# Kernel optimization log

Measured on AMD Instinct MI355X. Metric: run time of the kernel, lower is better.

## Reference

```python
import jax, jax.numpy as jnp
import numpy as np

N, F, H, CLS = 50000, 64, 128, 64   # nodes, node_features, second_features, num_classes
E, EL = 800000, 200000              # graph edges, decode (label) edges


def setup_inputs() -> dict:
    key = jax.random.key(0)
    ks = jax.random.split(key, 12)
    sc = lambda k, sh, fan: (jax.random.normal(k, sh, jnp.float32) / np.sqrt(fan)).astype(jnp.float32)
    return dict(
        x=jax.random.normal(ks[0], (N, F), jnp.float32),
        edge_index=jax.random.randint(ks[1], (2, E), 0, N),
        edge_label_index=jax.random.randint(ks[2], (2, EL), 0, N),
        hidden1=jnp.zeros((N, H), jnp.float32),   # H state of GCLSTM
        hidden2=jnp.zeros((N, H), jnp.float32),   # C state of GCLSTM
        # GCNConv params
        W_gcn=sc(ks[3], (F, F), F),
        b_gcn=jnp.zeros((F,), jnp.float32),
        # GCLSTM params, gates stacked along last axis in order (i, f, c, o)
        Wx=sc(ks[4], (F, 4 * H), F),      # input->gate weights W_i..W_o
        Th=sc(ks[5], (H, 4 * H), H),      # ChebConv(K=1) thetas on H (pure linear)
        b_gate=jnp.zeros((4 * H,), jnp.float32),  # b_i, b_f, b_c, b_o
        b_conv=jnp.zeros((4 * H,), jnp.float32),  # ChebConv biases
        w_c=sc(ks[6], (3, H), H),         # peephole w_c_i, w_c_f, w_c_o
        # output Linear
        W_lin=sc(ks[7], (H, CLS), H),
        b_lin=jnp.zeros((CLS,), jnp.float32),
    )


def _gcn(x, src, dst, W, b, n):
    """PyG GCNConv: add self-loops, symmetric D^-1/2 (A+I) D^-1/2 normalization."""
    xw = x @ W                                   # [N,F]
    loop = jnp.arange(n)
    src = jnp.concatenate([src, loop])
    dst = jnp.concatenate([dst, loop])
    deg = jax.ops.segment_sum(jnp.ones(src.shape, jnp.float32), dst, num_segments=n)
    dinv = jnp.where(deg > 0, jax.lax.rsqrt(deg), 0.0)
    norm = dinv[src] * dinv[dst]                 # [E+N]
    agg = jax.ops.segment_sum(norm[:, None] * xw[src], dst, num_segments=n)
    return agg + b


def reference(x, edge_index, edge_label_index, hidden1, hidden2,
              W_gcn, b_gcn, Wx, Th, b_gate, b_conv, w_c, W_lin, b_lin):
    n = x.shape[0]
    h = _gcn(x, edge_index[0], edge_index[1], W_gcn, b_gcn, n)   # GCNConv  [N,F]
    # GCLSTM, K=1: ChebConv on H degenerates to H @ Theta + b_conv
    g = (h @ Wx + b_gate) + (hidden1 @ Th + b_conv)              # [N,4H]
    gi, gf, gc, go = jnp.split(g, 4, axis=1)
    I = jax.nn.sigmoid(gi + w_c[0] * hidden2)
    Fg = jax.nn.sigmoid(gf + w_c[1] * hidden2)
    C = Fg * hidden2 + I * jnp.tanh(gc)
    O = jax.nn.sigmoid(go + w_c[2] * C)          # peephole on NEW cell state
    Hn = O * jnp.tanh(C)                         # [N,H]
    z = jax.nn.softmax(jax.nn.relu(Hn) @ W_lin + b_lin, axis=1)  # [N,CLS]
    # decode: dot product of endpoint embeddings
    r = jnp.sum(z[edge_label_index[0]] * z[edge_label_index[1]], axis=-1)  # [EL]
    # faithful to the original forward: returns input hidden1 and the NEW cell state
    return (r, hidden1, C)
```

## Files before the change

kernel.cpp:

```cpp
#include <hip/hip_runtime.h>
#include <math.h>

#define FDIM 64
#define HDIM 128
#define CLSD 64

#define NPART 8
#define MAXDEG 64

typedef unsigned short ushort_t;
typedef _Float16 hfrag __attribute__((ext_vector_type(8)));
typedef float f32x4 __attribute__((ext_vector_type(4)));

#define LOG2E 1.4426950408889634f

__device__ __forceinline__ float ex2(float x){ float r; asm("v_exp_f32 %0, %1" : "=v"(r) : "v"(x)); return r; }
__device__ __forceinline__ float rcp_(float x){ float r; asm("v_rcp_f32 %0, %1" : "=v"(r) : "v"(x)); return r; }
__device__ __forceinline__ float fsigmoid(float x){ return rcp_(1.0f + ex2(-LOG2E*x)); }
__device__ __forceinline__ float ftanh(float x){ return 1.0f - 2.0f*rcp_(1.0f + ex2(2.0f*LOG2E*x)); }

__device__ __forceinline__ ushort_t f2h(float f){
    _Float16 h = (_Float16)f;
    ushort_t u; __builtin_memcpy(&u, &h, 2); return u;
}
__device__ __forceinline__ float hflo(unsigned int u){
    ushort_t v = (ushort_t)u; _Float16 h; __builtin_memcpy(&h, &v, 2); return (float)h;
}
__device__ __forceinline__ float hfhi(unsigned int u){
    ushort_t v = (ushort_t)(u >> 16); _Float16 h; __builtin_memcpy(&h, &v, 2); return (float)h;
}
__device__ __forceinline__ unsigned int pk2h(float a, float b){
    return (unsigned int)f2h(a) | ((unsigned int)f2h(b) << 16);
}


__launch_bounds__(256)
__global__ void k_pre(const float* __restrict__ x,  const float* __restrict__ Wg,
                      const float* __restrict__ bg,
                      const float* __restrict__ Wx, const float* __restrict__ Th,
                      const float* __restrict__ Wl,
                      const float* __restrict__ bga, const float* __restrict__ bco,
                      const float* __restrict__ h1, const int* __restrict__ ei,
                      ushort_t* __restrict__ Bh, ushort_t* __restrict__ Lh,
                      float* __restrict__ bsum, int* __restrict__ cnt,
                      int* __restrict__ ell,
                      ushort_t* __restrict__ xh, ushort_t* __restrict__ Ab,
                      float* __restrict__ oh1, int N, int N2, int E, int psz,
                      int epBlocks){
    int t = threadIdx.x;
    if ((int)blockIdx.x < epBlocks){
        int p   = blockIdx.x % NPART;
        int bi  = blockIdx.x / NPART;
        int bpp = epBlocks / NPART;
        int chunk = (E + bpp - 1) / bpp;
        int beg = bi*chunk;
        int end = beg + chunk; if (end > E) end = E;
        int lo = p*psz, hi = lo + psz;
        for (int i = beg + t; i < end; i += 256){
            int d = ei[E + i];
            if (d >= lo && d < hi){
                int s = ei[i];
                int slot = atomicAdd(&cnt[d], 1);
                if (slot < MAXDEG) ell[(size_t)d*MAXDEG + slot] = s;
            }
        }
        return;
    }
    int tid = ((int)blockIdx.x - epBlocks)*256 + t;
    const int secX = 107008 + N*8;
    if (tid < 98304){
        int k = tid >> 9, col = tid & 511;
        float v;
        if (k < 64){
            float acc = 0.f;
            #pragma unroll 8
            for (int f = 0; f < 64; ++f) acc += Wg[k*64 + f]*Wx[f*512 + col];
            v = acc;
        } else {
            v = Th[(k-64)*512 + col];
        }
        int g = col >> 7, hc = col & 127;
        int w = hc >> 5, within = hc & 31;
        int c8 = g*2 + (within >> 4);
        int T = w*8 + c8;
        int s = k >> 5;
        int lane = ((k >> 3) & 3)*16 + (within & 15);
        int pos = ((T*6 + s)*64 + lane)*8 + (k & 7);
        Bh[pos] = f2h(v);
    } else if (tid < 106496){
        int i = tid - 98304;
        int k = i >> 6, col = i & 63;
        float v = Wl[k*64 + col];
        int ct = col >> 4;
        int s = k >> 5;
        int lane = ((k >> 3) & 3)*16 + (col & 15);
        int pos = ((ct*4 + s)*64 + lane)*8 + (k & 7);
        Lh[pos] = f2h(v);
    } else if (tid < 107008){
        int c = tid - 106496;
        float acc = bga[c] + bco[c];
        #pragma unroll 8
        for (int f = 0; f < 64; ++f) acc += bg[f]*Wx[f*512 + c];
        bsum[c] = acc;
    } else if (tid < secX){
        int i = tid - 107008;
        const float4* xp = (const float4*)(x + (size_t)i*8);
        float4 p0 = xp[0], p1 = xp[1];
        ((int4*)xh)[i] = make_int4((int)pk2h(p0.x,p0.y), (int)pk2h(p0.z,p0.w),
                                   (int)pk2h(p1.x,p1.y), (int)pk2h(p1.z,p1.w));
    } else {
        int i = tid - secX;
        if (i >= N2*16) return;
        int n = i >> 4, q = i & 15;
        int4 frag = make_int4(0,0,0,0);
        if (n < N){
            const float4* src = (const float4*)(h1 + (size_t)n*128 + q*8);
            float4 p0 = src[0], p1 = src[1];
            float4* dst = (float4*)(oh1 + (size_t)n*128 + q*8);
            dst[0] = p0; dst[1] = p1;
            frag = make_int4((int)pk2h(p0.x,p0.y), (int)pk2h(p0.z,p0.w),
                             (int)pk2h(p1.x,p1.y), (int)pk2h(p1.z,p1.w));
        }
        int s = 2 + (q >> 2);
        int lane = (q & 3)*16 + (n & 15);
        ((int4*)Ab)[((size_t)(n >> 4)*6 + s)*64 + lane] = frag;
    }
}

__launch_bounds__(256)
__global__ void k_gather(const int* __restrict__ cnt, const int* __restrict__ ell,
                         const ushort_t* __restrict__ xh,
                         ushort_t* __restrict__ Ab, int N, int N2){
    int tid = blockIdx.x*256 + threadIdx.x;
    int n = tid >> 3, q = tid & 7;
    if (n >= N2) return;
    int s_ = q >> 2;
    int lane = (q & 3)*16 + (n & 15);
    size_t fpos = ((size_t)(n >> 4)*6 + s_)*64 + lane;
    if (n >= N){
        ((int4*)Ab)[fpos] = make_int4(0,0,0,0);
        return;
    }
    int cn = cnt[n]; if (cn > MAXDEG) cn = MAXDEG;
    const int* row = ell + (size_t)n*MAXDEG;
    const int4* xv = (const int4*)xh;
    float a0=0.f,a1=0.f,a2=0.f,a3=0.f,a4=0.f,a5=0.f,a6=0.f,a7=0.f;
    int idx = 0;
    for (; idx + 4 <= cn; idx += 4){
        int s0 = row[idx], s1 = row[idx+1], s2 = row[idx+2], s3 = row[idx+3];
        float w0 = rsqrtf((float)cnt[s0] + 1.0f);
        float w1 = rsqrtf((float)cnt[s1] + 1.0f);
        float w2 = rsqrtf((float)cnt[s2] + 1.0f);
        float w3 = rsqrtf((float)cnt[s3] + 1.0f);
        int4 u = xv[(size_t)s0*8 + q];
        int4 p = xv[(size_t)s1*8 + q];
        int4 v = xv[(size_t)s2*8 + q];
        int4 z = xv[(size_t)s3*8 + q];
        a0 += w0*hflo((unsigned)u.x) + w1*hflo((unsigned)p.x) + w2*hflo((unsigned)v.x) + w3*hflo((unsigned)z.x);
        a1 += w0*hfhi((unsigned)u.x) + w1*hfhi((unsigned)p.x) + w2*hfhi((unsigned)v.x) + w3*hfhi((unsigned)z.x);
        a2 += w0*hflo((unsigned)u.y) + w1*hflo((unsigned)p.y) + w2*hflo((unsigned)v.y) + w3*hflo((unsigned)z.y);
        a3 += w0*hfhi((unsigned)u.y) + w1*hfhi((unsigned)p.y) + w2*hfhi((unsigned)v.y) + w3*hfhi((unsigned)z.y);
        a4 += w0*hflo((unsigned)u.z) + w1*hflo((unsigned)p.z) + w2*hflo((unsigned)v.z) + w3*hflo((unsigned)z.z);
        a5 += w0*hfhi((unsigned)u.z) + w1*hfhi((unsigned)p.z) + w2*hfhi((unsigned)v.z) + w3*hfhi((unsigned)z.z);
        a6 += w0*hflo((unsigned)u.w) + w1*hflo((unsigned)p.w) + w2*hflo((unsigned)v.w) + w3*hflo((unsigned)z.w);
        a7 += w0*hfhi((unsigned)u.w) + w1*hfhi((unsigned)p.w) + w2*hfhi((unsigned)v.w) + w3*hfhi((unsigned)z.w);
    }
    for (; idx < cn; ++idx){
        int s0 = row[idx];
        float w0 = rsqrtf((float)cnt[s0] + 1.0f);
        int4 u = xv[(size_t)s0*8 + q];
        a0 += w0*hflo((unsigned)u.x); a1 += w0*hfhi((unsigned)u.x);
        a2 += w0*hflo((unsigned)u.y); a3 += w0*hfhi((unsigned)u.y);
        a4 += w0*hflo((unsigned)u.z); a5 += w0*hfhi((unsigned)u.z);
        a6 += w0*hflo((unsigned)u.w); a7 += w0*hfhi((unsigned)u.w);
    }
    float dn = rsqrtf((float)cn + 1.0f);
    int4 sv = xv[(size_t)n*8 + q];
    a0 = dn*(a0 + dn*hflo((unsigned)sv.x));
    a1 = dn*(a1 + dn*hfhi((unsigned)sv.x));
    a2 = dn*(a2 + dn*hflo((unsigned)sv.y));
    a3 = dn*(a3 + dn*hfhi((unsigned)sv.y));
    a4 = dn*(a4 + dn*hflo((unsigned)sv.z));
    a5 = dn*(a5 + dn*hfhi((unsigned)sv.z));
    a6 = dn*(a6 + dn*hflo((unsigned)sv.w));
    a7 = dn*(a7 + dn*hfhi((unsigned)sv.w));
    ((int4*)Ab)[fpos] = make_int4((int)pk2h(a0,a1), (int)pk2h(a2,a3),
                                  (int)pk2h(a4,a5), (int)pk2h(a6,a7));
}

__launch_bounds__(256)
__global__ void k_fused(const ushort_t* __restrict__ Ab, const float* __restrict__ h2,
                        const ushort_t* __restrict__ Bh, const ushort_t* __restrict__ Lh,
                        const float* __restrict__ bsum, const float* __restrict__ wc,
                        const float* __restrict__ blin,
                        float* __restrict__ outC, ushort_t* __restrict__ zb, int N)
{
    __shared__ __align__(16) char smem[8448];
    ushort_t* Hh   = (ushort_t*)smem;
    float*    Ltile = (float*)(smem + 4096);

    const int t    = threadIdx.x;
    const int w    = t >> 6;
    const int lane = t & 63;
    const int nb   = blockIdx.x * 16;

    f32x4 acc[8];
    #pragma unroll
    for (int c8 = 0; c8 < 8; ++c8) acc[c8] = (f32x4){0.f,0.f,0.f,0.f};

    const hfrag* AF  = (const hfrag*)Ab;
    const hfrag* BhF = (const hfrag*)Bh;

    #pragma unroll
    for (int s = 0; s < 6; ++s){
        hfrag a0 = AF[((size_t)blockIdx.x*6 + s)*64 + lane];
        #pragma unroll
        for (int c8 = 0; c8 < 8; ++c8){
            int T = w*8 + c8;
            hfrag bh = BhF[(T*6 + s)*64 + lane];
            acc[c8] = __builtin_amdgcn_mfma_f32_16x16x32_f16(a0, bh, acc[c8], 0,0,0);
        }
    }

    #pragma unroll
    for (int hc_t = 0; hc_t < 2; ++hc_t){
        int hc  = w*32 + hc_t*16 + (lane & 15);
        float bi = bsum[hc],       bfv = bsum[128 + hc];
        float bc = bsum[256 + hc], bo  = bsum[384 + hc];
        float wci = wc[hc], wcf = wc[128 + hc], wco = wc[256 + hc];
        #pragma unroll
        for (int rr = 0; rr < 4; ++rr){
            int row = ((lane >> 4) & 3)*4 + rr;
            int gr  = nb + row;
            float gi = acc[0 + hc_t][rr] + bi;
            float gf = acc[2 + hc_t][rr] + bfv;
            float gc = acc[4 + hc_t][rr] + bc;
            float go = acc[6 + hc_t][rr] + bo;
            float hv = (gr < N) ? h2[(size_t)gr*128 + hc] : 0.0f;
            float I  = fsigmoid(gi + wci*hv);
            float Fg = fsigmoid(gf + wcf*hv);
            float C  = Fg*hv + I*ftanh(gc);
            float O  = fsigmoid(go + wco*C);
            float hn = O*ftanh(C);
            if (gr < N) outC[(size_t)gr*128 + hc] = C;
            float hr = fmaxf(hn, 0.0f);
            int l2  = row + (hc_t*2 + ((lane >> 3) & 1))*16;
            int pos = (w*64 + l2)*8 + (lane & 7);
            Hh[pos] = f2h(hr);
        }
    }
    __syncthreads();

    const hfrag* HF  = (const hfrag*)Hh;
    const hfrag* LhF = (const hfrag*)Lh;
    f32x4 acc2 = (f32x4){0.f,0.f,0.f,0.f};
    #pragma unroll
    for (int sp = 0; sp < 4; ++sp){
        hfrag a0 = HF[sp*64 + lane];
        hfrag bh = LhF[(w*4 + sp)*64 + lane];
        acc2 = __builtin_amdgcn_mfma_f32_16x16x32_f16(a0, bh, acc2, 0,0,0);
    }
    {
        int cls = w*16 + (lane & 15);
        float bv = blin[cls];
        #pragma unroll
        for (int rr = 0; rr < 4; ++rr){
            int row = ((lane >> 4) & 3)*4 + rr;
            Ltile[row*68 + cls] = acc2[rr] + bv;
        }
    }
    __syncthreads();

    {
        int m = t >> 4, q4 = t & 15;
        float4 v0 = *(const float4*)&Ltile[m*68 + q4*4];
        float mx = fmaxf(fmaxf(v0.x,v0.y), fmaxf(v0.z,v0.w));
        #pragma unroll
        for (int off2 = 1; off2 < 16; off2 <<= 1) mx = fmaxf(mx, __shfl_xor(mx, off2, 64));
        float e0 = ex2(LOG2E*(v0.x-mx)), e1 = ex2(LOG2E*(v0.y-mx));
        float e2 = ex2(LOG2E*(v0.z-mx)), e3 = ex2(LOG2E*(v0.w-mx));
        float s4 = e0+e1+e2+e3;
        #pragma unroll
        for (int off2 = 1; off2 < 16; off2 <<= 1) s4 += __shfl_xor(s4, off2, 64);
        float inv = rcp_(s4);
        if (nb + m < N){
            uint2 o; o.x = pk2h(e0*inv, e1*inv); o.y = pk2h(e2*inv, e3*inv);
            ((uint2*)zb)[(size_t)(nb+m)*16 + q4] = o;
        }
    }
}

__launch_bounds__(256)
__global__ void k_dec(const int* __restrict__ eli, const ushort_t* __restrict__ zb,
                      float* __restrict__ r, int EL){
    int tid = blockIdx.x*256 + threadIdx.x;
    int e = tid >> 3, l = tid & 7;
    if (e >= EL) return;
    int s = eli[e], d = eli[EL + e];
    int4 a = ((const int4*)zb)[(size_t)s*8 + l];
    int4 b = ((const int4*)zb)[(size_t)d*8 + l];
    unsigned int ua[4] = {(unsigned)a.x,(unsigned)a.y,(unsigned)a.z,(unsigned)a.w};
    unsigned int ub[4] = {(unsigned)b.x,(unsigned)b.y,(unsigned)b.z,(unsigned)b.w};
    float p = 0.f;
    #pragma unroll
    for (int j = 0; j < 4; ++j){
        p += hflo(ua[j])*hflo(ub[j]) + hfhi(ua[j])*hfhi(ub[j]);
    }
    #pragma unroll
    for (int off = 1; off < 8; off <<= 1) p += __shfl_xor(p, off, 64);
    if (l == 0) r[e] = p;
}

extern "C" void kernel_launch(void* const* d_in, const int* in_sizes, int n_in,
                              void* d_out, int out_size, void* d_ws, size_t ws_size,
                              hipStream_t stream)
{
    const float* x   = (const float*)d_in[0];
    const int*   ei  = (const int*)  d_in[1];
    const int*   eli = (const int*)  d_in[2];
    const float* h1  = (const float*)d_in[3];
    const float* h2  = (const float*)d_in[4];
    const float* Wg  = (const float*)d_in[5];
    const float* bg  = (const float*)d_in[6];
    const float* Wx  = (const float*)d_in[7];
    const float* Th  = (const float*)d_in[8];
    const float* bga = (const float*)d_in[9];
    const float* bco = (const float*)d_in[10];
    const float* wc  = (const float*)d_in[11];
    const float* Wl  = (const float*)d_in[12];
    const float* bl  = (const float*)d_in[13];

    const int N  = in_sizes[0] / FDIM;
    const int E  = in_sizes[1] / 2;
    const int EL = in_sizes[2] / 2;
    const int N2 = (N + 63) & ~63;
    const int PSZ = (N + NPART - 1) / NPART;

    float* ws   = (float*)d_ws;
    ushort_t* xh = (ushort_t*)ws;
    ushort_t* Ab = xh + (size_t)N*64;
    ushort_t* zb = Ab + (size_t)N2*192;
    int*   cnt  = (int*)(zb + (size_t)N*64);
    int*   ell  = cnt + N;
    size_t base = (size_t)((ell + (size_t)N*MAXDEG) - (int*)ws);
    base = (base + 3) & ~(size_t)3;
    ushort_t* Bh = (ushort_t*)(ws + base);
    ushort_t* Lh = Bh + 98304;
    float*  bsum = (float*)(Lh + 8192);

    float* out = (float*)d_out;
    float* r   = out;
    float* oh1 = out + EL;
    float* oC  = out + EL + (size_t)N*HDIM;

    const int epBlocks   = NPART * 256;
    const int preThreads = 107008 + N*8 + N2*16;
    const int preBlocks  = (preThreads + 255)/256;

    hipMemsetAsync(cnt, 0, (size_t)N*sizeof(int), stream);
    k_pre   <<<epBlocks + preBlocks, 256, 0, stream>>>(x, Wg, bg, Wx, Th, Wl, bga, bco,
                                                       h1, ei, Bh, Lh, bsum, cnt, ell,
                                                       xh, Ab, oh1, N, N2, E, PSZ,
                                                       epBlocks);
    k_gather<<<((size_t)N2*8 + 255)/256, 256, 0, stream>>>(cnt, ell, xh, Ab, N, N2);
    k_fused <<<N2/16, 256, 0, stream>>>(Ab, h2, Bh, Lh, bsum, wc, bl, oC, zb, N);
    k_dec   <<<(EL*8 + 255)/256, 256, 0, stream>>>(eli, zb, r, EL);
}
```

Baseline: 122.8 us.

## Fuse hidden1 conversion and copy into gate GEMM, split edge fill kernel

The hidden1 fp16 conversion and the copy of hidden1 to the output now happen inside the fused gate GEMM kernel, which loads h1 directly as MFMA A-fragments. This removes the intermediate fp16 Ab staging writes and reads for the hidden-state slices and shrinks the Ab buffer to the GCN part only. The ELL edge-fill work is split out of k_pre into its own kernel. This adds one more launch, and the fused kernel now does uncoalesced fp32 loads and conversions inside its MFMA loop.

```diff
diff --git a/kernel.cpp b/kernel.cpp
--- a/kernel.cpp
+++ b/kernel.cpp
@@ -40,34 +40,9 @@
                       const float* __restrict__ Wx, const float* __restrict__ Th,
                       const float* __restrict__ Wl,
                       const float* __restrict__ bga, const float* __restrict__ bco,
-                      const float* __restrict__ h1, const int* __restrict__ ei,
                       ushort_t* __restrict__ Bh, ushort_t* __restrict__ Lh,
-                      float* __restrict__ bsum, int* __restrict__ cnt,
-                      int* __restrict__ ell,
-                      ushort_t* __restrict__ xh, ushort_t* __restrict__ Ab,
-                      float* __restrict__ oh1, int N, int N2, int E, int psz,
-                      int epBlocks){
-    int t = threadIdx.x;
-    if ((int)blockIdx.x < epBlocks){
-        int p   = blockIdx.x % NPART;
-        int bi  = blockIdx.x / NPART;
-        int bpp = epBlocks / NPART;
-        int chunk = (E + bpp - 1) / bpp;
-        int beg = bi*chunk;
-        int end = beg + chunk; if (end > E) end = E;
-        int lo = p*psz, hi = lo + psz;
-        for (int i = beg + t; i < end; i += 256){
-            int d = ei[E + i];
-            if (d >= lo && d < hi){
-                int s = ei[i];
-                int slot = atomicAdd(&cnt[d], 1);
-                if (slot < MAXDEG) ell[(size_t)d*MAXDEG + slot] = s;
-            }
-        }
-        return;
-    }
-    int tid = ((int)blockIdx.x - epBlocks)*256 + t;
-    const int secX = 107008 + N*8;
+                      float* __restrict__ bsum, ushort_t* __restrict__ xh, int N){
+    int tid = blockIdx.x*256 + threadIdx.x;
     if (tid < 98304){
         int k = tid >> 9, col = tid & 511;
         float v;
@@ -102,28 +77,32 @@
         #pragma unroll 8
         for (int f = 0; f < 64; ++f) acc += bg[f]*Wx[f*512 + c];
         bsum[c] = acc;
-    } else if (tid < secX){
+    } else if (tid - 107008 < N*8){
         int i = tid - 107008;
         const float4* xp = (const float4*)(x + (size_t)i*8);
         float4 p0 = xp[0], p1 = xp[1];
         ((int4*)xh)[i] = make_int4((int)pk2h(p0.x,p0.y), (int)pk2h(p0.z,p0.w),
                                    (int)pk2h(p1.x,p1.y), (int)pk2h(p1.z,p1.w));
-    } else {
-        int i = tid - secX;
-        if (i >= N2*16) return;
-        int n = i >> 4, q = i & 15;
-        int4 frag = make_int4(0,0,0,0);
-        if (n < N){
-            const float4* src = (const float4*)(h1 + (size_t)n*128 + q*8);
-            float4 p0 = src[0], p1 = src[1];
-            float4* dst = (float4*)(oh1 + (size_t)n*128 + q*8);
-            dst[0] = p0; dst[1] = p1;
-            frag = make_int4((int)pk2h(p0.x,p0.y), (int)pk2h(p0.z,p0.w),
-                             (int)pk2h(p1.x,p1.y), (int)pk2h(p1.z,p1.w));
-        }
-        int s = 2 + (q >> 2);
-        int lane = (q & 3)*16 + (n & 15);
-        ((int4*)Ab)[((size_t)(n >> 4)*6 + s)*64 + lane] = frag;
+    }
+}
+
+__launch_bounds__(256)
+__global__ void k_fill(const int* __restrict__ ei, int* __restrict__ cnt,
+                       int* __restrict__ ell, int E, int psz){
+    int p   = blockIdx.x % NPART;
+    int bi  = blockIdx.x / NPART;
+    int bpp = gridDim.x / NPART;
+    int chunk = (E + bpp - 1) / bpp;
+    int beg = bi*chunk;
+    int end = beg + chunk; if (end > E) end = E;
+    int lo = p*psz, hi = lo + psz;
+    for (int i = beg + threadIdx.x; i < end; i += 256){
+        int d = ei[E + i];
+        if (d >= lo && d < hi){
+            int s = ei[i];
+            int slot = atomicAdd(&cnt[d], 1);
+            if (slot < MAXDEG) ell[(size_t)d*MAXDEG + slot] = s;
+        }
     }
 }
 
@@ -136,7 +115,7 @@
     if (n >= N2) return;
     int s_ = q >> 2;
     int lane = (q & 3)*16 + (n & 15);
-    size_t fpos = ((size_t)(n >> 4)*6 + s_)*64 + lane;
+    size_t fpos = ((size_t)(n >> 4)*2 + s_)*64 + lane;
     if (n >= N){
         ((int4*)Ab)[fpos] = make_int4(0,0,0,0);
         return;
@@ -189,11 +168,13 @@
 }
 
 __launch_bounds__(256)
-__global__ void k_fused(const ushort_t* __restrict__ Ab, const float* __restrict__ h2,
+__global__ void k_fused(const ushort_t* __restrict__ Ab, const float* __restrict__ h1,
+                        const float* __restrict__ h2,
                         const ushort_t* __restrict__ Bh, const ushort_t* __restrict__ Lh,
                         const float* __restrict__ bsum, const float* __restrict__ wc,
                         const float* __restrict__ blin,
-                        float* __restrict__ outC, ushort_t* __restrict__ zb, int N)
+                        float* __restrict__ outC, float* __restrict__ oh1,
+                        ushort_t* __restrict__ zb, int N)
 {
     __shared__ __align__(16) char smem[8448];
     ushort_t* Hh   = (ushort_t*)smem;
@@ -213,7 +194,25 @@
 
     #pragma unroll
     for (int s = 0; s < 6; ++s){
-        hfrag a0 = AF[((size_t)blockIdx.x*6 + s)*64 + lane];
+        hfrag a0;
+        if (s < 2){
+            a0 = AF[((size_t)blockIdx.x*2 + s)*64 + lane];
+        } else {
+            int gr = nb + (lane & 15);
+            int k1 = (s - 2)*32 + ((lane >> 4) & 3)*8;
+            float4 p0, p1;
+            if (gr < N){
+                const float4* src = (const float4*)(h1 + (size_t)gr*128 + k1);
+                p0 = src[0]; p1 = src[1];
+                float4* dst = (float4*)(oh1 + (size_t)gr*128 + k1);
+                dst[0] = p0; dst[1] = p1;
+            } else {
+                p0 = make_float4(0.f,0.f,0.f,0.f); p1 = p0;
+            }
+            unsigned int u[4] = {pk2h(p0.x,p0.y), pk2h(p0.z,p0.w),
+                                 pk2h(p1.x,p1.y), pk2h(p1.z,p1.w)};
+            __builtin_memcpy(&a0, u, 16);
+        }
         #pragma unroll
         for (int c8 = 0; c8 < 8; ++c8){
             int T = w*8 + c8;
@@ -339,7 +338,7 @@
     float* ws   = (float*)d_ws;
     ushort_t* xh = (ushort_t*)ws;
     ushort_t* Ab = xh + (size_t)N*64;
-    ushort_t* zb = Ab + (size_t)N2*192;
+    ushort_t* zb = Ab + (size_t)N2*64;
     int*   cnt  = (int*)(zb + (size_t)N*64);
     int*   ell  = cnt + N;
     size_t base = (size_t)((ell + (size_t)N*MAXDEG) - (int*)ws);
@@ -353,16 +352,15 @@
     float* oh1 = out + EL;
     float* oC  = out + EL + (size_t)N*HDIM;
 
+    const int preThreads = 107008 + N*8;
     const int epBlocks   = NPART * 256;
-    const int preThreads = 107008 + N*8 + N2*16;
-    const int preBlocks  = (preThreads + 255)/256;
 
     hipMemsetAsync(cnt, 0, (size_t)N*sizeof(int), stream);
-    k_pre   <<<epBlocks + preBlocks, 256, 0, stream>>>(x, Wg, bg, Wx, Th, Wl, bga, bco,
-                                                       h1, ei, Bh, Lh, bsum, cnt, ell,
-                                                       xh, Ab, oh1, N, N2, E, PSZ,
-                                                       epBlocks);
+    k_pre   <<<(preThreads + 255)/256, 256, 0, stream>>>(x, Wg, bg, Wx, Th, Wl, bga, bco,
+                                                         Bh, Lh, bsum, xh, N);
+    k_fill  <<<epBlocks, 256, 0, stream>>>(ei, cnt, ell, E, PSZ);
     k_gather<<<((size_t)N2*8 + 255)/256, 256, 0, stream>>>(cnt, ell, xh, Ab, N, N2);
-    k_fused <<<N2/16, 256, 0, stream>>>(Ab, h2, Bh, Lh, bsum, wc, bl, oC, zb, N);
+    k_fused <<<N2/16, 256, 0, stream>>>(Ab, h1, h2, Bh, Lh, bsum, wc, bl,
+                                        oC, oh1, zb, N);
     k_dec   <<<(EL*8 + 255)/256, 256, 0, stream>>>(eli, zb, r, EL);
 }
```

New measurement: 137.2 us. +11.7%, slower.
